# Kernel optimization log

Measured on AMD Instinct MI355X. Metric: run time of the kernel, lower is better.

The kernel has to match this reference:

```python
import jax, jax.numpy as jnp
import numpy as np

B, S, F, L = 512, 1024, 64, 128  # batch, seq_len, n_features, latent_dim


def _lstm_cell(x_t, h, c, W_ih, W_hh, b):
    # PyTorch gate order: i, f, g, o. W_ih: [4L, F], W_hh: [4L, L], b: [4L]
    g = x_t @ W_ih.T + h @ W_hh.T + b
    i, f, gg, o = jnp.split(g, 4, axis=-1)
    c_new = jax.nn.sigmoid(f) * c + jax.nn.sigmoid(i) * jnp.tanh(gg)
    h_new = jax.nn.sigmoid(o) * jnp.tanh(c_new)
    return h_new, c_new


def setup_inputs() -> dict:
    key = jax.random.key(0)
    ks = jax.random.split(key, 12)
    sF = 1.0 / np.sqrt(F)
    sL = 1.0 / np.sqrt(L)
    return {
        "x": jax.random.normal(ks[0], (B, S, F), dtype=jnp.float32),
        # encoder LSTM (single layer)
        "W_ih_enc": jax.random.uniform(ks[1], (4 * L, F), jnp.float32, -sL, sL),
        "W_hh_enc": jax.random.uniform(ks[2], (4 * L, L), jnp.float32, -sL, sL),
        "b_ih_enc": jax.random.uniform(ks[3], (4 * L,), jnp.float32, -sL, sL),
        "b_hh_enc": jax.random.uniform(ks[4], (4 * L,), jnp.float32, -sL, sL),
        # decoder LSTMCell
        "W_ih_dec": jax.random.uniform(ks[5], (4 * L, F), jnp.float32, -sL, sL),
        "W_hh_dec": jax.random.uniform(ks[6], (4 * L, L), jnp.float32, -sL, sL),
        "b_ih_dec": jax.random.uniform(ks[7], (4 * L,), jnp.float32, -sL, sL),
        "b_hh_dec": jax.random.uniform(ks[8], (4 * L,), jnp.float32, -sL, sL),
        # decoder dense: Linear(latent_dim, n_features)
        "W_dense": jax.random.uniform(ks[9], (F, L), jnp.float32, -sL, sL),
        "b_dense": jax.random.uniform(ks[10], (F,), jnp.float32, -sL, sL),
    }


def reference(x, W_ih_enc, W_hh_enc, b_ih_enc, b_hh_enc,
              W_ih_dec, W_hh_dec, b_ih_dec, b_hh_dec, W_dense, b_dense):
    Bn, Sn, Fn = x.shape
    b_enc = b_ih_enc + b_hh_enc
    b_dec = b_ih_dec + b_hh_dec

    # ---- encoder: single-layer LSTM, batch_first; keep only (h_n, c_n) ----
    def enc_step(carry, x_t):
        h, c = carry
        h, c = _lstm_cell(x_t, h, c, W_ih_enc, W_hh_enc, b_enc)
        return (h, c), None

    h0 = jnp.zeros((Bn, L), x.dtype)
    c0 = jnp.zeros((Bn, L), x.dtype)
    (h_n, c_n), _ = jax.lax.scan(enc_step, (h0, c0), jnp.swapaxes(x, 0, 1))

    x0 = h_n @ W_dense.T + b_dense  # dense_dec1(h_i[0]) before the loop

    def dec_step(carry, _):
        h, c, x_i = carry
        h, c = _lstm_cell(x_i, h, c, W_ih_dec, W_hh_dec, b_dec)
        x_i = h @ W_dense.T + b_dense
        return (h, c, x_i), x_i

    _, outs = jax.lax.scan(dec_step, (h_n, c_n, x0), None, length=Sn)
    out = jnp.swapaxes(outs, 0, 1)  # [B, S, F]
    return jnp.flip(out, axis=1)    # torch.flip(out, [1])
```

## Files before the change

kernel.cpp:

```cpp
#include <hip/hip_runtime.h>

constexpr int Bn = 512;
constexpr int Sn = 1024;
constexpr int Fn = 64;
constexpr int Ln = 128;
constexpr int Gn = 4 * Ln;
constexpr int CH = 16;
constexpr int NCH = Sn / CH;
constexpr int XST = 44;
constexpr int PST = 1028;
constexpr int HST = 80;

typedef unsigned int u32;
typedef _Float16 h2 __attribute__((ext_vector_type(2)));
typedef _Float16 h8 __attribute__((ext_vector_type(8)));
typedef float f4 __attribute__((ext_vector_type(4)));

__device__ __forceinline__ float fsig(float v) {
  return __builtin_amdgcn_rcpf(1.0f + __expf(-v));
}
__device__ __forceinline__ h8 as_h8(uint4 v) { return __builtin_bit_cast(h8, v); }

__global__ void pack_kernel(const float* __restrict__ Wih, const float* __restrict__ Whh,
                            const float* __restrict__ Wd,
                            _Float16* __restrict__ WhE, _Float16* __restrict__ WxE,
                            _Float16* __restrict__ WdH) {
  const int i = blockIdx.x * 256 + threadIdx.x;
  if (i < Gn * Ln) WhE[i] = (_Float16)Whh[i];
  if (i < Gn * Fn) WxE[i] = (_Float16)Wih[i];
  if (i < Fn * Ln) WdH[i] = (_Float16)Wd[i];
}

__global__ void combine_dec_kernel(const float* __restrict__ Wih, const float* __restrict__ Whh,
                                   const float* __restrict__ bih, const float* __restrict__ bhh,
                                   const float* __restrict__ Wd, const float* __restrict__ bd,
                                   _Float16* __restrict__ WcH, float* __restrict__ bc) {
  const int t = blockIdx.x;
  const int l = threadIdx.x;
  float s = Whh[t * Ln + l];
#pragma unroll
  for (int j = 0; j < Fn; ++j) s += Wih[t * Fn + j] * Wd[j * Ln + l];
  WcH[t * Ln + l] = (_Float16)s;
  if (l == 0) {
    float sb = bih[t] + bhh[t];
#pragma unroll
    for (int j = 0; j < Fn; ++j) sb += Wih[t * Fn + j] * bd[j];
    bc[t] = sb;
  }
}

__global__ __launch_bounds__(512)
void rae_mfma3_kernel(const float* __restrict__ x,
                      const _Float16* __restrict__ WhE, const _Float16* __restrict__ WxE,
                      const float* __restrict__ bih_e, const float* __restrict__ bhh_e,
                      const _Float16* __restrict__ WcH, const float* __restrict__ bc,
                      const _Float16* __restrict__ WdH, const float* __restrict__ bd,
                      float* __restrict__ out) {
  const int t = threadIdx.x;
  const int w = t >> 6;
  const int l = t & 63;
  const int jj = l & 15;
  const int g16 = l >> 4;
  const int b = blockIdx.x;

  __shared__ float pre[CH * PST];
  __shared__ u32 xraw[2 * CH * XST];
  __shared__ u32 hsb[2 * 2 * HST];

  uint4 bh[4][4];
  float be[4];
#pragma unroll
  for (int g = 0; g < 4; ++g) {
    const int row = (w + 8 * g) * 16 + jj;
#pragma unroll
    for (int kt = 0; kt < 4; ++kt)
      bh[g][kt] = *(const uint4*)(WhE + (size_t)row * 128 + kt * 32 + g16 * 8);
    be[g] = bih_e[row] + bhh_e[row];
  }

  float c = 0.0f;

  for (int i = t; i < 2 * 2 * HST; i += 512) hsb[i] = 0u;

  const int se = t >> 8, sst = (t >> 4) & 15, sfq = t & 15;
  const float* xsrc = x + (size_t)b * 2 * Sn * Fn + (size_t)se * Sn * Fn +
                      (size_t)sst * Fn + sfq * 4;
  float4 xv = *(const float4*)xsrc;
  __syncthreads();

  int s = 0;
  for (int ch = 0; ch < NCH; ++ch) {
    {
      h2 p0 = {(_Float16)xv.x, (_Float16)xv.y};
      h2 p1 = {(_Float16)xv.z, (_Float16)xv.w};
      xraw[se * (CH * XST) + sst * XST + sfq * 2] = __builtin_bit_cast(u32, p0);
      xraw[se * (CH * XST) + sst * XST + sfq * 2 + 1] = __builtin_bit_cast(u32, p1);
    }
    __syncthreads();
    {
      uint4 bx0[4], bx1[4];
#pragma unroll
      for (int g = 0; g < 4; ++g) {
        const int row = (w + 8 * g) * 16 + jj;
        bx0[g] = *(const uint4*)(WxE + (size_t)row * 64 + g16 * 8);
        bx1[g] = *(const uint4*)(WxE + (size_t)row * 64 + 32 + g16 * 8);
      }
#pragma unroll
      for (int mt = 0; mt < 2; ++mt) {
        h8 a0 = as_h8(*(const uint4*)&xraw[mt * (CH * XST) + jj * XST + g16 * 4]);
        h8 a1 = as_h8(*(const uint4*)&xraw[mt * (CH * XST) + jj * XST + 16 + g16 * 4]);
#pragma unroll
        for (int g = 0; g < 4; ++g) {
          f4 acc = {be[g], be[g], be[g], be[g]};
          acc = __builtin_amdgcn_mfma_f32_16x16x32_f16(a0, as_h8(bx0[g]), acc, 0, 0, 0);
          acc = __builtin_amdgcn_mfma_f32_16x16x32_f16(a1, as_h8(bx1[g]), acc, 0, 0, 0);
          const int col = (w + 8 * g) * 16 + jj;
#pragma unroll
          for (int r = 0; r < 4; ++r)
            pre[(g16 * 4 + r) * PST + mt * 514 + col] = acc[r];
        }
      }
    }
    if (ch + 1 < NCH)
      xv = *(const float4*)(xsrc + (size_t)(ch + 1) * CH * Fn);
    __syncthreads();
    for (int ss = 0; ss < CH; ++ss, ++s) {
      const int cur = s & 1, nx = cur ^ 1;
      const u32* hb = &hsb[(cur * 2 + (jj & 1)) * HST];
      f4 a0 = {0.f, 0.f, 0.f, 0.f}, a1 = a0, a2 = a0, a3 = a0;
#pragma unroll
      for (int kt = 0; kt < 4; ++kt) {
        h8 af = as_h8(*(const uint4*)&hb[kt * 16 + g16 * 4]);
        a0 = __builtin_amdgcn_mfma_f32_16x16x32_f16(af, as_h8(bh[0][kt]), a0, 0, 0, 0);
        a1 = __builtin_amdgcn_mfma_f32_16x16x32_f16(af, as_h8(bh[1][kt]), a1, 0, 0, 0);
        a2 = __builtin_amdgcn_mfma_f32_16x16x32_f16(af, as_h8(bh[2][kt]), a2, 0, 0, 0);
        a3 = __builtin_amdgcn_mfma_f32_16x16x32_f16(af, as_h8(bh[3][kt]), a3, 0, 0, 0);
      }
      if (l < 32) {
        const int e = g16;
        const float* pp = &pre[ss * PST + e * 514];
        const float pi = pp[(w + 0) * 16 + jj];
        const float pf = pp[(w + 8) * 16 + jj];
        const float pg = pp[(w + 16) * 16 + jj];
        const float po = pp[(w + 24) * 16 + jj];
        const float gi = fsig((e ? a0[1] : a0[0]) + pi);
        const float gf = fsig((e ? a1[1] : a1[0]) + pf);
        const float gg = __builtin_fmaf(2.f, fsig(2.f * ((e ? a2[1] : a2[0]) + pg)), -1.f);
        const float go = fsig((e ? a3[1] : a3[0]) + po);
        c = __builtin_fmaf(gf, c, gi * gg);
        ((_Float16*)hsb)[(nx * 2 + e) * (2 * HST) + w * 16 + jj] =
            (_Float16)(go * __builtin_fmaf(2.f, fsig(2.f * c), -1.f));
      }
      __syncthreads();
    }
  }

  float bdv[4];
#pragma unroll
  for (int g = 0; g < 4; ++g) {
    const int row = (w + 8 * g) * 16 + jj;
#pragma unroll
    for (int kt = 0; kt < 4; ++kt)
      bh[g][kt] = *(const uint4*)(WcH + (size_t)row * 128 + kt * 32 + g16 * 8);
    bdv[g] = bc[row];
  }
  uint4 dwf[4];
  float dbias = 0.0f;
  const int od = w * 16 + jj;
  if (w < 4) {
#pragma unroll
    for (int kt = 0; kt < 4; ++kt)
      dwf[kt] = *(const uint4*)(WdH + (size_t)od * 128 + kt * 32 + g16 * 8);
    dbias = bd[od];
  }
  float* outb = out + (size_t)b * 2 * Sn * Fn;

  for (int step = 0; step < Sn; ++step, ++s) {
    const int cur = s & 1, nx = cur ^ 1;
    const u32* hb = &hsb[(cur * 2 + (jj & 1)) * HST];
    f4 a0 = {bdv[0], bdv[0], bdv[0], bdv[0]};
    f4 a1 = {bdv[1], bdv[1], bdv[1], bdv[1]};
    f4 a2 = {bdv[2], bdv[2], bdv[2], bdv[2]};
    f4 a3 = {bdv[3], bdv[3], bdv[3], bdv[3]};
#pragma unroll
    for (int kt = 0; kt < 4; ++kt) {
      h8 af = as_h8(*(const uint4*)&hb[kt * 16 + g16 * 4]);
      a0 = __builtin_amdgcn_mfma_f32_16x16x32_f16(af, as_h8(bh[0][kt]), a0, 0, 0, 0);
      a1 = __builtin_amdgcn_mfma_f32_16x16x32_f16(af, as_h8(bh[1][kt]), a1, 0, 0, 0);
      a2 = __builtin_amdgcn_mfma_f32_16x16x32_f16(af, as_h8(bh[2][kt]), a2, 0, 0, 0);
      a3 = __builtin_amdgcn_mfma_f32_16x16x32_f16(af, as_h8(bh[3][kt]), a3, 0, 0, 0);
    }
    if (l < 32) {
      const int e = g16;
      const float gi = fsig(e ? a0[1] : a0[0]);
      const float gf = fsig(e ? a1[1] : a1[0]);
      const float gg = __builtin_fmaf(2.f, fsig(2.f * (e ? a2[1] : a2[0])), -1.f);
      const float go = fsig(e ? a3[1] : a3[0]);
      c = __builtin_fmaf(gf, c, gi * gg);
      ((_Float16*)hsb)[(nx * 2 + e) * (2 * HST) + w * 16 + jj] =
          (_Float16)(go * __builtin_fmaf(2.f, fsig(2.f * c), -1.f));
    }
    __syncthreads();

    if (w < 4) {
      const u32* hn = &hsb[(nx * 2 + (jj & 1)) * HST];
      f4 d = {0.f, 0.f, 0.f, 0.f};
#pragma unroll
      for (int kt = 0; kt < 4; ++kt) {
        h8 af = as_h8(*(const uint4*)&hn[kt * 16 + g16 * 4]);
        d = __builtin_amdgcn_mfma_f32_16x16x32_f16(af, as_h8(dwf[kt]), d, 0, 0, 0);
      }
      if (l < 16) {
        const size_t roff = (size_t)(Sn - 1 - step) * Fn + w * 16 + l;
        outb[roff] = d[0] + dbias;
        outb[(size_t)Sn * Fn + roff] = d[1] + dbias;
      }
    }
  }
}

extern "C" void kernel_launch(void* const* d_in, const int* in_sizes, int n_in,
                              void* d_out, int out_size, void* d_ws, size_t ws_size,
                              hipStream_t stream) {
  const float* x     = (const float*)d_in[0];
  const float* Wih_e = (const float*)d_in[1];
  const float* Whh_e = (const float*)d_in[2];
  const float* bih_e = (const float*)d_in[3];
  const float* bhh_e = (const float*)d_in[4];
  const float* Wih_d = (const float*)d_in[5];
  const float* Whh_d = (const float*)d_in[6];
  const float* bih_d = (const float*)d_in[7];
  const float* bhh_d = (const float*)d_in[8];
  const float* Wd    = (const float*)d_in[9];
  const float* bd    = (const float*)d_in[10];
  float* out = (float*)d_out;

  _Float16* WhE = (_Float16*)d_ws;
  _Float16* WxE = WhE + Gn * Ln;
  _Float16* WcH = WxE + Gn * Fn;
  _Float16* WdH = WcH + Gn * Ln;
  float* bc = (float*)(WdH + Fn * Ln);

  pack_kernel<<<256, 256, 0, stream>>>(Wih_e, Whh_e, Wd, WhE, WxE, WdH);
  combine_dec_kernel<<<Gn, Ln, 0, stream>>>(Wih_d, Whh_d, bih_d, bhh_d, Wd, bd, WcH, bc);
  rae_mfma3_kernel<<<Bn / 2, 512, 0, stream>>>(x, WhE, WxE, bih_e, bhh_e,
                                               WcH, bc, WdH, bd, out);
}
```

Baseline: 1.193 ms.

## Split LSTM gate math across half-waves and use LDS-only barriers

Gate nonlinearities are now split across both half-waves: lanes 0-31 compute the i/f gates and lanes 32-63 the g/o gates, and the results are exchanged with a lane shuffle, which halves the serial transcendental work per step. __syncthreads is replaced by a barrier that waits only on LDS counters, so in-flight global loads (the next x chunk prefetch) are not forced to drain at every step. The encoder's precomputed input projections are prefetched one step ahead into registers. The cost is extra shuffles and select logic, and the correctness of the lighter barrier depends on the outstanding global loads not being needed before the next barrier.

```diff
diff --git a/kernel.cpp b/kernel.cpp
--- a/kernel.cpp
+++ b/kernel.cpp
@@ -21,6 +21,12 @@
 }
 __device__ __forceinline__ h8 as_h8(uint4 v) { return __builtin_bit_cast(h8, v); }
 
+__device__ __forceinline__ void lgkm_barrier() {
+  asm volatile("s_waitcnt lgkmcnt(0)" ::: "memory");
+  __builtin_amdgcn_s_barrier();
+  asm volatile("" ::: "memory");
+}
+
 __global__ void pack_kernel(const float* __restrict__ Wih, const float* __restrict__ Whh,
                             const float* __restrict__ Wd,
                             _Float16* __restrict__ WhE, _Float16* __restrict__ WxE,
@@ -50,7 +56,7 @@
 }
 
 __global__ __launch_bounds__(512)
-void rae_mfma3_kernel(const float* __restrict__ x,
+void rae_mfma4_kernel(const float* __restrict__ x,
                       const _Float16* __restrict__ WhE, const _Float16* __restrict__ WxE,
                       const float* __restrict__ bih_e, const float* __restrict__ bhh_e,
                       const _Float16* __restrict__ WcH, const float* __restrict__ bc,
@@ -61,7 +67,13 @@
   const int l = t & 63;
   const int jj = l & 15;
   const int g16 = l >> 4;
+  const bool low = l < 32;
+  const int e = g16 & 1;
   const int b = blockIdx.x;
+
+  const float m1 = low ? 1.0f : 2.0f;
+  const float ad1 = low ? 0.0f : -1.0f;
+  const int gA = low ? 0 : 2, gB = low ? 1 : 3;
 
   __shared__ float pre[CH * PST];
   __shared__ u32 xraw[2 * CH * XST];
@@ -87,6 +99,9 @@
                       (size_t)sst * Fn + sfq * 4;
   float4 xv = *(const float4*)xsrc;
   __syncthreads();
+
+  const int pofA = e * 514 + (w + 8 * gA) * 16 + jj;
+  const int pofB = e * 514 + (w + 8 * gB) * 16 + jj;
 
   int s = 0;
   for (int ch = 0; ch < NCH; ++ch) {
@@ -96,7 +111,7 @@
       xraw[se * (CH * XST) + sst * XST + sfq * 2] = __builtin_bit_cast(u32, p0);
       xraw[se * (CH * XST) + sst * XST + sfq * 2 + 1] = __builtin_bit_cast(u32, p1);
     }
-    __syncthreads();
+    lgkm_barrier();
     {
       uint4 bx0[4], bx1[4];
 #pragma unroll
@@ -123,7 +138,8 @@
     }
     if (ch + 1 < NCH)
       xv = *(const float4*)(xsrc + (size_t)(ch + 1) * CH * Fn);
-    __syncthreads();
+    lgkm_barrier();
+    float pA = pre[pofA], pB = pre[pofB];
     for (int ss = 0; ss < CH; ++ss, ++s) {
       const int cur = s & 1, nx = cur ^ 1;
       const u32* hb = &hsb[(cur * 2 + (jj & 1)) * HST];
@@ -136,22 +152,21 @@
         a2 = __builtin_amdgcn_mfma_f32_16x16x32_f16(af, as_h8(bh[2][kt]), a2, 0, 0, 0);
         a3 = __builtin_amdgcn_mfma_f32_16x16x32_f16(af, as_h8(bh[3][kt]), a3, 0, 0, 0);
       }
-      if (l < 32) {
-        const int e = g16;
-        const float* pp = &pre[ss * PST + e * 514];
-        const float pi = pp[(w + 0) * 16 + jj];
-        const float pf = pp[(w + 8) * 16 + jj];
-        const float pg = pp[(w + 16) * 16 + jj];
-        const float po = pp[(w + 24) * 16 + jj];
-        const float gi = fsig((e ? a0[1] : a0[0]) + pi);
-        const float gf = fsig((e ? a1[1] : a1[0]) + pf);
-        const float gg = __builtin_fmaf(2.f, fsig(2.f * ((e ? a2[1] : a2[0]) + pg)), -1.f);
-        const float go = fsig((e ? a3[1] : a3[0]) + po);
-        c = __builtin_fmaf(gf, c, gi * gg);
-        ((_Float16*)hsb)[(nx * 2 + e) * (2 * HST) + w * 16 + jj] =
-            (_Float16)(go * __builtin_fmaf(2.f, fsig(2.f * c), -1.f));
-      }
-      __syncthreads();
+      const int ssn = (ss + 1 < CH) ? ss + 1 : ss;
+      const float pAn = pre[ssn * PST + pofA];
+      const float pBn = pre[ssn * PST + pofB];
+      const float sel1 = low ? (e ? a0[1] : a0[0]) : (e ? a2[1] : a2[0]);
+      const float sel2 = low ? (e ? a1[1] : a1[0]) : (e ? a3[1] : a3[0]);
+      const float g1 = __builtin_fmaf(m1, fsig(m1 * (sel1 + pA)), ad1);
+      const float g2 = fsig(sel2 + pB);
+      const float gg = __shfl_xor(g1, 32, 64);
+      const float go = __shfl_xor(g2, 32, 64);
+      c = __builtin_fmaf(g2, c, g1 * gg);
+      const float tc = __builtin_fmaf(2.f, fsig(2.f * c), -1.f);
+      if (low)
+        ((_Float16*)hsb)[(nx * 2 + e) * (2 * HST) + w * 16 + jj] = (_Float16)(go * tc);
+      lgkm_barrier();
+      pA = pAn; pB = pBn;
     }
   }
 
@@ -190,17 +205,17 @@
       a2 = __builtin_amdgcn_mfma_f32_16x16x32_f16(af, as_h8(bh[2][kt]), a2, 0, 0, 0);
       a3 = __builtin_amdgcn_mfma_f32_16x16x32_f16(af, as_h8(bh[3][kt]), a3, 0, 0, 0);
     }
-    if (l < 32) {
-      const int e = g16;
-      const float gi = fsig(e ? a0[1] : a0[0]);
-      const float gf = fsig(e ? a1[1] : a1[0]);
-      const float gg = __builtin_fmaf(2.f, fsig(2.f * (e ? a2[1] : a2[0])), -1.f);
-      const float go = fsig(e ? a3[1] : a3[0]);
-      c = __builtin_fmaf(gf, c, gi * gg);
-      ((_Float16*)hsb)[(nx * 2 + e) * (2 * HST) + w * 16 + jj] =
-          (_Float16)(go * __builtin_fmaf(2.f, fsig(2.f * c), -1.f));
-    }
-    __syncthreads();
+    const float sel1 = low ? (e ? a0[1] : a0[0]) : (e ? a2[1] : a2[0]);
+    const float sel2 = low ? (e ? a1[1] : a1[0]) : (e ? a3[1] : a3[0]);
+    const float g1 = __builtin_fmaf(m1, fsig(m1 * sel1), ad1);
+    const float g2 = fsig(sel2);
+    const float gg = __shfl_xor(g1, 32, 64);
+    const float go = __shfl_xor(g2, 32, 64);
+    c = __builtin_fmaf(g2, c, g1 * gg);
+    const float tc = __builtin_fmaf(2.f, fsig(2.f * c), -1.f);
+    if (low)
+      ((_Float16*)hsb)[(nx * 2 + e) * (2 * HST) + w * 16 + jj] = (_Float16)(go * tc);
+    lgkm_barrier();
 
     if (w < 4) {
       const u32* hn = &hsb[(nx * 2 + (jj & 1)) * HST];
@@ -243,6 +258,6 @@
 
   pack_kernel<<<256, 256, 0, stream>>>(Wih_e, Whh_e, Wd, WhE, WxE, WdH);
   combine_dec_kernel<<<Gn, Ln, 0, stream>>>(Wih_d, Whh_d, bih_d, bhh_d, Wd, bd, WcH, bc);
-  rae_mfma3_kernel<<<Bn / 2, 512, 0, stream>>>(x, WhE, WxE, bih_e, bhh_e,
+  rae_mfma4_kernel<<<Bn / 2, 512, 0, stream>>>(x, WhE, WxE, bih_e, bhh_e,
                                                WcH, bc, WdH, bd, out);
 }
```

Measured after the change: 1.300 ms. +8.9%, slower.
